# Optimization experiments

Measured on AMD Instinct MI355X. Metric: run time of the kernel, lower is better.

The kernel has to match this reference:

```python
import jax, jax.numpy as jnp
import numpy as np

HID = 1024
HEADS = 16
HEAD_DIM = HID // HEADS
FFN = 4096
EPS = 1e-5


def setup_inputs() -> dict:
    key = jax.random.key(0)
    ks = jax.random.split(key, 12)
    s = lambda k, shape, fan_in: jax.random.normal(k, shape, jnp.float32) * (fan_in ** -0.5)
    return {
        "hidden_states": jax.random.normal(ks[0], (2, 2048, HID), jnp.float32),
        "Wq": s(ks[1], (HID, HID), HID),
        "Wk": s(ks[2], (HID, HID), HID),
        "Wv": s(ks[3], (HID, HID), HID),
        "Wo": s(ks[4], (HID, HID), HID),
        "W1": s(ks[5], (HID, FFN), HID),
        "b1": jnp.zeros((FFN,), jnp.float32),
        "W2": s(ks[6], (FFN, HID), FFN),
        "b2": jnp.zeros((HID,), jnp.float32),
        "ln1_scale": jnp.ones((HID,), jnp.float32),
        "ln1_shift": jnp.zeros((HID,), jnp.float32),
        "ln2_scale": jnp.ones((HID,), jnp.float32),
        "ln2_shift": jnp.zeros((HID,), jnp.float32),
    }


def _layer_norm(x, scale, shift):
    mean = jnp.mean(x, axis=-1, keepdims=True)
    var = jnp.var(x, axis=-1, keepdims=True)  # biased, matches unbiased=False
    return (x - mean) * jax.lax.rsqrt(var + EPS) * scale + shift


def _forward(hidden_states, Wq, Wk, Wv, Wo, W1, b1, W2, b2,
             ln1_scale, ln1_shift, ln2_scale, ln2_shift):
    bsz, seq_len, _ = hidden_states.shape
    residual = hidden_states
    x = _layer_norm(hidden_states, ln1_scale, ln1_shift)

    # q/k/v projections -> [b, h, s, d]
    def proj(W):
        return (x @ W).reshape(bsz, seq_len, HEADS, HEAD_DIM).transpose(0, 2, 1, 3)
    q, k, v = proj(Wq), proj(Wk), proj(Wv)

    scores = jnp.einsum("bhqd,bhkd->bhqk", q, k)
    causal = jnp.triu(jnp.ones((seq_len, seq_len), bool), k=1)
    scores = jnp.where(causal, -jnp.inf, scores) / (HEAD_DIM ** 0.5)
    attn = jax.nn.softmax(scores, axis=-1)  # dropout is identity in eval
    out = jnp.einsum("bhqk,bhkd->bhqd", attn, v)
    out = out.transpose(0, 2, 1, 3).reshape(bsz, seq_len, HID)
    hidden_states = residual + out @ Wo

    residual = hidden_states
    y = _layer_norm(hidden_states, ln2_scale, ln2_shift)
    y = jax.nn.gelu(y @ W1 + b1, approximate=False) @ W2 + b2  # torch nn.GELU default = exact erf
    return residual + y


def reference(hidden_states, Wq, Wk, Wv, Wo, W1, b1, W2, b2,
              ln1_scale, ln1_shift, ln2_scale, ln2_shift):
    return _forward(hidden_states, Wq, Wk, Wv, Wo, W1, b1, W2, b2,
                    ln1_scale, ln1_shift, ln2_scale, ln2_shift)
```

## Files before the change

kernel.cpp:

```cpp
#include <hip/hip_runtime.h>
#include <math.h>

using bf16x8 = __attribute__((ext_vector_type(8))) short;
using f32x4  = __attribute__((ext_vector_type(4))) float;

struct __align__(8) us4 { unsigned short x, y, z, w; };

__device__ __forceinline__ unsigned short f2b(float f) {
  union { float f; unsigned u; } v; v.f = f;
  unsigned r = v.u + 0x7FFFu + ((v.u >> 16) & 1u);
  return (unsigned short)(r >> 16);
}

#define GLDS(g, l) __builtin_amdgcn_global_load_lds(                        \
    (const __attribute__((address_space(1))) void*)(g),                    \
    (__attribute__((address_space(3))) void*)(l), 16, 0, 0)

__global__ void __launch_bounds__(256) transpose_w(
    const float* __restrict__ src, unsigned short* __restrict__ dst,
    int K, int N) {
  __shared__ float tile[32][33];
  const int n0 = blockIdx.x * 32, k0 = blockIdx.y * 32;
  const int tx = threadIdx.x & 31, ty = threadIdx.x >> 5;
#pragma unroll
  for (int i = 0; i < 32; i += 8)
    tile[ty + i][tx] = src[(size_t)(k0 + ty + i) * N + n0 + tx];
  __syncthreads();
#pragma unroll
  for (int i = 0; i < 32; i += 8)
    dst[(size_t)(n0 + ty + i) * K + k0 + tx] = f2b(tile[tx][ty + i]);
}

__global__ void __launch_bounds__(256) ln_kernel(
    const float* __restrict__ in, const float* __restrict__ scale,
    const float* __restrict__ shift, unsigned short* __restrict__ out) {
  const int row = blockIdx.x, t = threadIdx.x;
  const float4 v = ((const float4*)(in + (size_t)row * 1024))[t];
  float s  = v.x + v.y + v.z + v.w;
  float s2 = v.x * v.x + v.y * v.y + v.z * v.z + v.w * v.w;
#pragma unroll
  for (int off = 32; off; off >>= 1) {
    s  += __shfl_xor(s,  off);
    s2 += __shfl_xor(s2, off);
  }
  __shared__ float red[8];
  const int w = t >> 6, lane = t & 63;
  if (!lane) { red[w] = s; red[4 + w] = s2; }
  __syncthreads();
  s  = red[0] + red[1] + red[2] + red[3];
  s2 = red[4] + red[5] + red[6] + red[7];
  const float mean = s * (1.0f / 1024.0f);
  const float var  = s2 * (1.0f / 1024.0f) - mean * mean;
  const float rstd = rsqrtf(var + 1e-5f);
  const float4 sc = ((const float4*)scale)[t];
  const float4 sh = ((const float4*)shift)[t];
  us4 o;
  o.x = f2b((v.x - mean) * rstd * sc.x + sh.x);
  o.y = f2b((v.y - mean) * rstd * sc.y + sh.y);
  o.z = f2b((v.z - mean) * rstd * sc.z + sh.z);
  o.w = f2b((v.w - mean) * rstd * sc.w + sh.w);
  ((us4*)(out + (size_t)row * 1024))[t] = o;
}

template <int MODE>
__global__ void __launch_bounds__(512, 2) gemm256(
    const unsigned short* __restrict__ A, const unsigned short* __restrict__ B,
    int K, int N, unsigned short* __restrict__ outb,
    const float* __restrict__ bias, unsigned short* __restrict__ vt) {
  __shared__ unsigned short lA[2][256 * 64];
  __shared__ unsigned short lB[2][256 * 64];
  const int t = threadIdx.x, lane = t & 63;
  const int w = t >> 6, wm = w >> 2, wn = w & 3;
  const int r16 = lane & 15, g = lane >> 4;
  const int m0 = blockIdx.x * 256, n0 = blockIdx.y * 256;

  const unsigned short* aSrc[4];
  const unsigned short* bSrc[4];
#pragma unroll
  for (int p = 0; p < 4; ++p) {
    const int ci = t + p * 512, r = ci >> 3, cs = ci & 7;
    aSrc[p] = A + (size_t)(m0 + r) * K + (cs ^ (r & 7)) * 8;
    bSrc[p] = B + (size_t)(n0 + r) * K + (cs ^ (r & 7)) * 8;
  }
  int aOff[8][2], bOff[4][2];
#pragma unroll
  for (int i = 0; i < 8; ++i)
#pragma unroll
    for (int ks = 0; ks < 2; ++ks) {
      const int m = wm * 128 + i * 16 + r16, kb = ks * 4 + g;
      aOff[i][ks] = ((m << 3) + (kb ^ (m & 7))) << 3;
    }
#pragma unroll
  for (int j = 0; j < 4; ++j)
#pragma unroll
    for (int ks = 0; ks < 2; ++ks) {
      const int n = wn * 64 + j * 16 + r16, kb = ks * 4 + g;
      bOff[j][ks] = ((n << 3) + (kb ^ (n & 7))) << 3;
    }

  auto stage = [&](int buf, int kt) {
    const int off = kt * 64;
#pragma unroll
    for (int p = 0; p < 4; ++p) {
      GLDS(aSrc[p] + off, &lA[buf][(t + p * 512) * 8]);
      GLDS(bSrc[p] + off, &lB[buf][(t + p * 512) * 8]);
    }
  };

  f32x4 acc[8][4] = {};
  const int nkt = K >> 6;
  stage(0, 0);
  for (int kt = 0; kt < nkt; ++kt) {
    const int cur = kt & 1;
    if (kt + 1 < nkt) {
      stage(cur ^ 1, kt + 1);
      asm volatile("s_waitcnt vmcnt(8)" ::: "memory");
    } else {
      asm volatile("s_waitcnt vmcnt(0)" ::: "memory");
    }
    __builtin_amdgcn_s_barrier();
    __builtin_amdgcn_sched_barrier(0);
    const unsigned short* bA = lA[cur];
    const unsigned short* bB = lB[cur];
#pragma unroll
    for (int ks = 0; ks < 2; ++ks) {
      bf16x8 af[8], bfr[4];
#pragma unroll
      for (int i = 0; i < 8; ++i) af[i] = *(const bf16x8*)&bA[aOff[i][ks]];
#pragma unroll
      for (int j = 0; j < 4; ++j) bfr[j] = *(const bf16x8*)&bB[bOff[j][ks]];
      __builtin_amdgcn_s_setprio(1);
#pragma unroll
      for (int i = 0; i < 8; ++i)
#pragma unroll
        for (int j = 0; j < 4; ++j)
          acc[i][j] = __builtin_amdgcn_mfma_f32_16x16x32_bf16(
              af[i], bfr[j], acc[i][j], 0, 0, 0);
      __builtin_amdgcn_s_setprio(0);
    }
    __builtin_amdgcn_sched_barrier(0);
    __builtin_amdgcn_s_barrier();
  }

  float bj[4];
  if constexpr (MODE == 2) {
#pragma unroll
    for (int j = 0; j < 4; ++j) bj[j] = bias[n0 + wn * 64 + j * 16 + r16];
  }
#pragma unroll
  for (int i = 0; i < 8; ++i) {
    const int row0 = m0 + wm * 128 + i * 16 + g * 4;
#pragma unroll
    for (int j = 0; j < 4; ++j) {
      const int colb = n0 + wn * 64 + j * 16;
      const int col = colb + r16;
      if constexpr (MODE == 0) {
        if (colb < 2048) {
#pragma unroll
          for (int r = 0; r < 4; ++r)
            outb[(size_t)(row0 + r) * 2048 + col] = f2b(acc[i][j][r]);
        } else {
          const int b = row0 >> 11, s0 = row0 & 2047;
          us4 pk;
          pk.x = f2b(acc[i][j][0]); pk.y = f2b(acc[i][j][1]);
          pk.z = f2b(acc[i][j][2]); pk.w = f2b(acc[i][j][3]);
          *(us4*)&vt[((size_t)b * 1024 + (col - 2048)) * 2048 + s0] = pk;
        }
      } else {
#pragma unroll
        for (int r = 0; r < 4; ++r) {
          const float x = acc[i][j][r] + bj[j];
          const float u = x * (0.7978845608028654f + 0.03567740814f * x * x);
          const float e = __builtin_amdgcn_exp2f(u * 2.885390081777927f);
          const float th = 1.0f - 2.0f * __builtin_amdgcn_rcpf(e + 1.0f);
          outb[(size_t)(row0 + r) * N + col] = f2b(0.5f * x * (1.0f + th));
        }
      }
    }
  }
}

template <int MODE, int BM>
__global__ void __launch_bounds__(256) gemm_bt(
    const unsigned short* __restrict__ A, const unsigned short* __restrict__ B,
    int K, int N,
    float* __restrict__ outf, const float* __restrict__ bias,
    const float* __restrict__ resid) {
  constexpr int WN = (BM == 128) ? 2 : 4;
  constexpr int NJ = 128 / (16 * WN);
  constexpr int ACH = BM / 32;
  __shared__ unsigned short lA[2][BM * 64];
  __shared__ unsigned short lB[2][128 * 64];
  const int t = threadIdx.x, lane = t & 63;
  const int w = t >> 6, wm = w / WN, wn = w % WN;
  const int r16 = lane & 15, g = lane >> 4;
  const int m0 = blockIdx.x * BM, n0 = blockIdx.y * 128;

  const unsigned short* aSrc[ACH];
  const unsigned short* bSrc[4];
#pragma unroll
  for (int p = 0; p < ACH; ++p) {
    const int ci = t + p * 256, m = ci >> 3, cs = ci & 7;
    aSrc[p] = A + (size_t)(m0 + m) * K + (cs ^ (m & 7)) * 8;
  }
#pragma unroll
  for (int p = 0; p < 4; ++p) {
    const int ci = t + p * 256, m = ci >> 3, cs = ci & 7;
    bSrc[p] = B + (size_t)(n0 + m) * K + (cs ^ (m & 7)) * 8;
  }

  int aOff[4][2], bOff[NJ][2];
#pragma unroll
  for (int i = 0; i < 4; ++i)
#pragma unroll
    for (int ks = 0; ks < 2; ++ks) {
      const int m = wm * 64 + i * 16 + r16, kb = ks * 4 + g;
      aOff[i][ks] = ((m << 3) + (kb ^ (m & 7))) << 3;
    }
#pragma unroll
  for (int j = 0; j < NJ; ++j)
#pragma unroll
    for (int ks = 0; ks < 2; ++ks) {
      const int n = wn * (16 * NJ) + j * 16 + r16, kb = ks * 4 + g;
      bOff[j][ks] = ((n << 3) + (kb ^ (n & 7))) << 3;
    }

  auto stage = [&](int buf, int kt) {
    const int off = kt * 64;
#pragma unroll
    for (int p = 0; p < ACH; ++p)
      GLDS(aSrc[p] + off, &lA[buf][(t + p * 256) * 8]);
#pragma unroll
    for (int p = 0; p < 4; ++p)
      GLDS(bSrc[p] + off, &lB[buf][(t + p * 256) * 8]);
  };

  f32x4 acc[4][NJ] = {};
  const int nkt = K >> 6;
  stage(0, 0);
  __syncthreads();
  for (int kt = 0; kt < nkt; ++kt) {
    const int cur = kt & 1;
    if (kt + 1 < nkt) stage(cur ^ 1, kt + 1);
    const unsigned short* bA = lA[cur];
    const unsigned short* bB = lB[cur];
#pragma unroll
    for (int ks = 0; ks < 2; ++ks) {
      bf16x8 af[4], bfr[NJ];
#pragma unroll
      for (int i = 0; i < 4; ++i) af[i] = *(const bf16x8*)&bA[aOff[i][ks]];
#pragma unroll
      for (int j = 0; j < NJ; ++j) bfr[j] = *(const bf16x8*)&bB[bOff[j][ks]];
#pragma unroll
      for (int i = 0; i < 4; ++i)
#pragma unroll
        for (int j = 0; j < NJ; ++j)
          acc[i][j] = __builtin_amdgcn_mfma_f32_16x16x32_bf16(
              af[i], bfr[j], acc[i][j], 0, 0, 0);
    }
    __syncthreads();
  }

  float bj[NJ];
  if constexpr (MODE == 3) {
#pragma unroll
    for (int j = 0; j < NJ; ++j)
      bj[j] = bias[n0 + wn * (16 * NJ) + j * 16 + r16];
  }
#pragma unroll
  for (int i = 0; i < 4; ++i) {
    const int row0 = m0 + wm * 64 + i * 16 + g * 4;
#pragma unroll
    for (int j = 0; j < NJ; ++j) {
      const int col = n0 + wn * (16 * NJ) + j * 16 + r16;
      if constexpr (MODE == 1) {
#pragma unroll
        for (int r = 0; r < 4; ++r) {
          const size_t idx = (size_t)(row0 + r) * N + col;
          outf[idx] = acc[i][j][r] + resid[idx];
        }
      } else {
#pragma unroll
        for (int r = 0; r < 4; ++r) {
          const size_t idx = (size_t)(row0 + r) * N + col;
          outf[idx] = acc[i][j][r] + bj[j] + resid[idx];
        }
      }
    }
  }
}

__global__ void __launch_bounds__(256) attn_kernel(
    const unsigned short* __restrict__ qk, const unsigned short* __restrict__ vt,
    unsigned short* __restrict__ obuf) {
  const int j = blockIdx.x, h = blockIdx.y, bb = blockIdx.z;
  const int t = threadIdx.x, lane = t & 63, w = t >> 6;
  const int r16 = lane & 15, g = lane >> 4;
  __shared__ unsigned short lK[2][64 * 64];
  __shared__ unsigned short lV[2][64 * 64];
  __shared__ unsigned short lP[4][16 * 72];

  const int qtA = j, qtB = 31 - j;
  const int ktmax = qtB;
  const int qrowA = qtA * 64 + w * 16 + r16;
  const int qrowB = qtB * 64 + w * 16 + r16;
  const float CE = 0.18033688011112042f;

  bf16x8 qfA[2], qfB[2];
  {
    const unsigned short* qa =
        qk + (size_t)(bb * 2048 + qrowA) * 2048 + h * 64;
    qfA[0] = *(const bf16x8*)(qa + g * 8);
    qfA[1] = *(const bf16x8*)(qa + 32 + g * 8);
    const unsigned short* qb =
        qk + (size_t)(bb * 2048 + qrowB) * 2048 + h * 64;
    qfB[0] = *(const bf16x8*)(qb + g * 8);
    qfB[1] = *(const bf16x8*)(qb + 32 + g * 8);
  }

  f32x4 accA[4] = {}, accB[4] = {};
  float mA = -3.0e38f, lA_ = 0.0f, mB = -3.0e38f, lB_ = 0.0f;

  auto stage = [&](int buf, int kt) {
    const int k0 = kt * 64;
#pragma unroll
    for (int p = 0; p < 2; ++p) {
      const int ci = t + p * 256;
      const int r = ci >> 3, cs = ci & 7;
      const int cb = cs ^ (r & 7);
      GLDS(qk + (size_t)(bb * 2048 + k0 + r) * 2048 + 1024 + h * 64 + cb * 8,
           &lK[buf][ci * 8]);
      GLDS(vt + ((size_t)bb * 1024 + h * 64 + r) * 2048 + k0 + cb * 8,
           &lV[buf][ci * 8]);
    }
  };

  auto flash_step = [&](const bf16x8* qf, f32x4* accO, float& mrun,
                        float& lrun, int qrow, bool diag, int k0, int cur) {
    f32x4 s[4] = {};
#pragma unroll
    for (int ks = 0; ks < 2; ++ks)
#pragma unroll
      for (int mt = 0; mt < 4; ++mt) {
        const int r = mt * 16 + r16, db = ks * 4 + g;
        const bf16x8 kf =
            *(const bf16x8*)&lK[cur][((r << 3) + (db ^ (r & 7))) << 3];
        s[mt] = __builtin_amdgcn_mfma_f32_16x16x32_bf16(kf, qf[ks], s[mt],
                                                        0, 0, 0);
      }
    if (diag) {
#pragma unroll
      for (int mt = 0; mt < 4; ++mt)
#pragma unroll
        for (int r = 0; r < 4; ++r)
          if (k0 + mt * 16 + g * 4 + r > qrow) s[mt][r] = -3.0e38f;
    }
    float tmax = -3.0e38f;
#pragma unroll
    for (int mt = 0; mt < 4; ++mt)
#pragma unroll
      for (int r = 0; r < 4; ++r) tmax = fmaxf(tmax, s[mt][r]);
    tmax = fmaxf(tmax, __shfl_xor(tmax, 16));
    tmax = fmaxf(tmax, __shfl_xor(tmax, 32));
    const float mnew = fmaxf(mrun, tmax);
    const float fac = __builtin_amdgcn_exp2f((mrun - mnew) * CE);
    float pv[4][4];
    float tsum = 0.0f;
#pragma unroll
    for (int mt = 0; mt < 4; ++mt)
#pragma unroll
      for (int r = 0; r < 4; ++r) {
        pv[mt][r] = __builtin_amdgcn_exp2f((s[mt][r] - mnew) * CE);
        tsum += pv[mt][r];
      }
    tsum += __shfl_xor(tsum, 16);
    tsum += __shfl_xor(tsum, 32);
    lrun = lrun * fac + tsum;
    mrun = mnew;
#pragma unroll
    for (int mt = 0; mt < 4; ++mt) {
      us4 pk;
      pk.x = f2b(pv[mt][0]); pk.y = f2b(pv[mt][1]);
      pk.z = f2b(pv[mt][2]); pk.w = f2b(pv[mt][3]);
      *(us4*)&lP[w][r16 * 72 + mt * 16 + g * 4] = pk;
    }
    float fr[4];
#pragma unroll
    for (int r = 0; r < 4; ++r) fr[r] = __shfl(fac, g * 4 + r);
#pragma unroll
    for (int nb = 0; nb < 4; ++nb)
#pragma unroll
      for (int r = 0; r < 4; ++r) accO[nb][r] *= fr[r];
#pragma unroll
    for (int ks = 0; ks < 2; ++ks) {
      const bf16x8 pa = *(const bf16x8*)&lP[w][r16 * 72 + ks * 32 + g * 8];
#pragma unroll
      for (int nb = 0; nb < 4; ++nb) {
        const int d = nb * 16 + r16, kb = ks * 4 + g;
        const bf16x8 vf =
            *(const bf16x8*)&lV[cur][((d << 3) + (kb ^ (d & 7))) << 3];
        accO[nb] = __builtin_amdgcn_mfma_f32_16x16x32_bf16(pa, vf, accO[nb],
                                                           0, 0, 0);
      }
    }
  };

  stage(0, 0);
  __syncthreads();
  int cur = 0;
  for (int kt = 0; kt <= ktmax; ++kt) {
    if (kt < ktmax) stage(cur ^ 1, kt + 1);
    flash_step(qfB, accB, mB, lB_, qrowB, kt == qtB, kt * 64, cur);
    if (kt <= qtA)
      flash_step(qfA, accA, mA, lA_, qrowA, kt == qtA, kt * 64, cur);
    __syncthreads();
    cur ^= 1;
  }

  auto epilogue = [&](const f32x4* accO, float lrun, int q0) {
    const float li = 1.0f / lrun;
    float lr_[4];
#pragma unroll
    for (int r = 0; r < 4; ++r) lr_[r] = __shfl(li, g * 4 + r);
#pragma unroll
    for (int nb = 0; nb < 4; ++nb)
#pragma unroll
      for (int r = 0; r < 4; ++r) {
        const int row = bb * 2048 + q0 + w * 16 + g * 4 + r;
        const int col = h * 64 + nb * 16 + r16;
        obuf[(size_t)row * 1024 + col] = f2b(accO[nb][r] * lr_[r]);
      }
  };
  epilogue(accA, lA_, qtA * 64);
  epilogue(accB, lB_, qtB * 64);
}

extern "C" void kernel_launch(void* const* d_in, const int* in_sizes, int n_in,
                              void* d_out, int out_size, void* d_ws,
                              size_t ws_size, hipStream_t stream) {
  const float* hs   = (const float*)d_in[0];
  const float* Wq   = (const float*)d_in[1];
  const float* Wk   = (const float*)d_in[2];
  const float* Wv   = (const float*)d_in[3];
  const float* Wo   = (const float*)d_in[4];
  const float* W1   = (const float*)d_in[5];
  const float* b1   = (const float*)d_in[6];
  const float* W2   = (const float*)d_in[7];
  const float* b2   = (const float*)d_in[8];
  const float* ln1s = (const float*)d_in[9];
  const float* ln1b = (const float*)d_in[10];
  const float* ln2s = (const float*)d_in[11];
  const float* ln2b = (const float*)d_in[12];
  float* out = (float*)d_out;

  char* ws = (char*)d_ws;
  unsigned short* wqkvT = (unsigned short*)(ws + 0);
  unsigned short* woT   = (unsigned short*)(ws + 6291456);
  unsigned short* w1T   = (unsigned short*)(ws + 8388608);
  unsigned short* w2T   = (unsigned short*)(ws + 16777216);
  float*          hid   = (float*)(ws + 25165824);
  unsigned short* xb    = (unsigned short*)(ws + 41943040);
  char*           big   = ws + 50331648;
  unsigned short* qkb   = (unsigned short*)(big);
  unsigned short* vtb   = (unsigned short*)(big + 16777216);
  unsigned short* ob    = (unsigned short*)(big + 25165824);
  unsigned short* h1    = (unsigned short*)(big);

  transpose_w<<<dim3(32, 32), 256, 0, stream>>>(Wq, wqkvT, 1024, 1024);
  transpose_w<<<dim3(32, 32), 256, 0, stream>>>(Wk, wqkvT + 1024 * 1024, 1024, 1024);
  transpose_w<<<dim3(32, 32), 256, 0, stream>>>(Wv, wqkvT + 2 * 1024 * 1024, 1024, 1024);
  transpose_w<<<dim3(32, 32), 256, 0, stream>>>(Wo, woT, 1024, 1024);
  transpose_w<<<dim3(128, 32), 256, 0, stream>>>(W1, w1T, 1024, 4096);
  transpose_w<<<dim3(32, 128), 256, 0, stream>>>(W2, w2T, 4096, 1024);

  ln_kernel<<<4096, 256, 0, stream>>>(hs, ln1s, ln1b, xb);
  gemm256<0><<<dim3(16, 12), 512, 0, stream>>>(xb, wqkvT, 1024, 3072,
                                               qkb, nullptr, vtb);
  attn_kernel<<<dim3(16, 16, 2), 256, 0, stream>>>(qkb, vtb, ob);
  gemm_bt<1, 64><<<dim3(64, 8), 256, 0, stream>>>(ob, woT, 1024, 1024,
                                                  hid, nullptr, hs);
  ln_kernel<<<4096, 256, 0, stream>>>(hid, ln2s, ln2b, xb);
  gemm256<2><<<dim3(16, 16), 512, 0, stream>>>(xb, w1T, 1024, 4096,
                                               h1, b1, nullptr);
  gemm_bt<3, 64><<<dim3(64, 8), 256, 0, stream>>>(h1, w2T, 4096, 1024,
                                                  out, b2, hid);
}
```

Baseline: 247.0 us.

## Tune GEMM sync with vmcnt waits, lazy softmax rescale, packed bf16 convert, swizzled P

The GEMM loop drops the full __syncthreads in favour of explicit vmcnt waits plus a raw s_barrier, so the next tile's loads can stay in flight, and it raises wave priority around the MFMA blocks. In attention, the online-softmax rescale now runs only when some row's max grows by more than a threshold, which skips the accumulator multiply in most steps. P is converted with the hardware packed bf16 instruction and stored to an XOR-swizzled 64-wide LDS buffer instead of a padded 72-wide one. These are several independent tweaks. The threshold-based lazy rescale, the hand-counted vmcnt values and the inline asm all carry correctness risk.

After: 242.7 us. No clear change (-1.7%).

```diff
diff --git a/kernel.cpp b/kernel.cpp
--- a/kernel.cpp
+++ b/kernel.cpp
@@ -5,11 +5,17 @@
 using f32x4  = __attribute__((ext_vector_type(4))) float;
 
 struct __align__(8) us4 { unsigned short x, y, z, w; };
+struct __align__(8) u32x2 { unsigned int x, y; };
 
 __device__ __forceinline__ unsigned short f2b(float f) {
   union { float f; unsigned u; } v; v.f = f;
   unsigned r = v.u + 0x7FFFu + ((v.u >> 16) & 1u);
   return (unsigned short)(r >> 16);
+}
+__device__ __forceinline__ unsigned int cvt_pk_bf16(float lo, float hi) {
+  unsigned int d;
+  asm("v_cvt_pk_bf16_f32 %0, %1, %2" : "=v"(d) : "v"(lo), "v"(hi));
+  return d;
 }
 
 #define GLDS(g, l) __builtin_amdgcn_global_load_lds(                        \
@@ -238,10 +244,19 @@
   f32x4 acc[4][NJ] = {};
   const int nkt = K >> 6;
   stage(0, 0);
-  __syncthreads();
   for (int kt = 0; kt < nkt; ++kt) {
     const int cur = kt & 1;
-    if (kt + 1 < nkt) stage(cur ^ 1, kt + 1);
+    if (kt + 1 < nkt) {
+      stage(cur ^ 1, kt + 1);
+      if constexpr (ACH == 2)
+        asm volatile("s_waitcnt vmcnt(6)" ::: "memory");
+      else
+        asm volatile("s_waitcnt vmcnt(8)" ::: "memory");
+    } else {
+      asm volatile("s_waitcnt vmcnt(0)" ::: "memory");
+    }
+    __builtin_amdgcn_s_barrier();
+    __builtin_amdgcn_sched_barrier(0);
     const unsigned short* bA = lA[cur];
     const unsigned short* bB = lB[cur];
 #pragma unroll
@@ -251,14 +266,17 @@
       for (int i = 0; i < 4; ++i) af[i] = *(const bf16x8*)&bA[aOff[i][ks]];
 #pragma unroll
       for (int j = 0; j < NJ; ++j) bfr[j] = *(const bf16x8*)&bB[bOff[j][ks]];
+      __builtin_amdgcn_s_setprio(1);
 #pragma unroll
       for (int i = 0; i < 4; ++i)
 #pragma unroll
         for (int j = 0; j < NJ; ++j)
           acc[i][j] = __builtin_amdgcn_mfma_f32_16x16x32_bf16(
               af[i], bfr[j], acc[i][j], 0, 0, 0);
-    }
-    __syncthreads();
+      __builtin_amdgcn_s_setprio(0);
+    }
+    __builtin_amdgcn_sched_barrier(0);
+    __builtin_amdgcn_s_barrier();
   }
 
   float bj[NJ];
@@ -298,7 +316,7 @@
   const int r16 = lane & 15, g = lane >> 4;
   __shared__ unsigned short lK[2][64 * 64];
   __shared__ unsigned short lV[2][64 * 64];
-  __shared__ unsigned short lP[4][16 * 72];
+  __shared__ unsigned short lP[4][16 * 64];
 
   const int qtA = j, qtB = 31 - j;
   const int ktmax = qtB;
@@ -308,12 +326,10 @@
 
   bf16x8 qfA[2], qfB[2];
   {
-    const unsigned short* qa =
-        qk + (size_t)(bb * 2048 + qrowA) * 2048 + h * 64;
+    const unsigned short* qa = qk + (size_t)(bb * 2048 + qrowA) * 2048 + h * 64;
     qfA[0] = *(const bf16x8*)(qa + g * 8);
     qfA[1] = *(const bf16x8*)(qa + 32 + g * 8);
-    const unsigned short* qb =
-        qk + (size_t)(bb * 2048 + qrowB) * 2048 + h * 64;
+    const unsigned short* qb = qk + (size_t)(bb * 2048 + qrowB) * 2048 + h * 64;
     qfB[0] = *(const bf16x8*)(qb + g * 8);
     qfB[1] = *(const bf16x8*)(qb + 32 + g * 8);
   }
@@ -335,9 +351,12 @@
     }
   };
 
+  const int pswz = (r16 & 7) << 3;
+
   auto flash_step = [&](const bf16x8* qf, f32x4* accO, float& mrun,
                         float& lrun, int qrow, bool diag, int k0, int cur) {
     f32x4 s[4] = {};
+    __builtin_amdgcn_s_setprio(1);
 #pragma unroll
     for (int ks = 0; ks < 2; ++ks)
 #pragma unroll
@@ -348,6 +367,7 @@
         s[mt] = __builtin_amdgcn_mfma_f32_16x16x32_bf16(kf, qf[ks], s[mt],
                                                         0, 0, 0);
       }
+    __builtin_amdgcn_s_setprio(0);
     if (diag) {
 #pragma unroll
       for (int mt = 0; mt < 4; ++mt)
@@ -362,38 +382,43 @@
       for (int r = 0; r < 4; ++r) tmax = fmaxf(tmax, s[mt][r]);
     tmax = fmaxf(tmax, __shfl_xor(tmax, 16));
     tmax = fmaxf(tmax, __shfl_xor(tmax, 32));
-    const float mnew = fmaxf(mrun, tmax);
-    const float fac = __builtin_amdgcn_exp2f((mrun - mnew) * CE);
+    if (!__all(tmax <= mrun + 44.0f)) {
+      const float mnew = fmaxf(mrun, tmax);
+      const float fac = __builtin_amdgcn_exp2f((mrun - mnew) * CE);
+      lrun *= fac;
+      float fr[4];
+#pragma unroll
+      for (int r = 0; r < 4; ++r) fr[r] = __shfl(fac, g * 4 + r);
+#pragma unroll
+      for (int nb = 0; nb < 4; ++nb)
+#pragma unroll
+        for (int r = 0; r < 4; ++r) accO[nb][r] *= fr[r];
+      mrun = mnew;
+    }
     float pv[4][4];
     float tsum = 0.0f;
 #pragma unroll
     for (int mt = 0; mt < 4; ++mt)
 #pragma unroll
       for (int r = 0; r < 4; ++r) {
-        pv[mt][r] = __builtin_amdgcn_exp2f((s[mt][r] - mnew) * CE);
+        pv[mt][r] = __builtin_amdgcn_exp2f((s[mt][r] - mrun) * CE);
         tsum += pv[mt][r];
       }
     tsum += __shfl_xor(tsum, 16);
     tsum += __shfl_xor(tsum, 32);
-    lrun = lrun * fac + tsum;
-    mrun = mnew;
+    lrun += tsum;
 #pragma unroll
     for (int mt = 0; mt < 4; ++mt) {
-      us4 pk;
-      pk.x = f2b(pv[mt][0]); pk.y = f2b(pv[mt][1]);
-      pk.z = f2b(pv[mt][2]); pk.w = f2b(pv[mt][3]);
-      *(us4*)&lP[w][r16 * 72 + mt * 16 + g * 4] = pk;
-    }
-    float fr[4];
-#pragma unroll
-    for (int r = 0; r < 4; ++r) fr[r] = __shfl(fac, g * 4 + r);
-#pragma unroll
-    for (int nb = 0; nb < 4; ++nb)
-#pragma unroll
-      for (int r = 0; r < 4; ++r) accO[nb][r] *= fr[r];
-#pragma unroll
-    for (int ks = 0; ks < 2; ++ks) {
-      const bf16x8 pa = *(const bf16x8*)&lP[w][r16 * 72 + ks * 32 + g * 8];
+      u32x2 pk;
+      pk.x = cvt_pk_bf16(pv[mt][0], pv[mt][1]);
+      pk.y = cvt_pk_bf16(pv[mt][2], pv[mt][3]);
+      *(u32x2*)&lP[w][r16 * 64 + ((mt * 16 + g * 4) ^ pswz)] = pk;
+    }
+    __builtin_amdgcn_s_setprio(1);
+#pragma unroll
+    for (int ks = 0; ks < 2; ++ks) {
+      const bf16x8 pa =
+          *(const bf16x8*)&lP[w][r16 * 64 + ((ks * 32 + g * 8) ^ pswz)];
 #pragma unroll
       for (int nb = 0; nb < 4; ++nb) {
         const int d = nb * 16 + r16, kb = ks * 4 + g;
@@ -403,6 +428,7 @@
                                                            0, 0, 0);
       }
     }
+    __builtin_amdgcn_s_setprio(0);
   };
 
   stage(0, 0);
```
